# Kernel tuning notes

Hardware: AMD Instinct MI355X
Metric: run time of the kernel (lower is better)

The kernel has to match this reference:

```python
import jax, jax.numpy as jnp
import numpy as np

B, S, D = 8, 1024, 768          # batch, block_size, d_model
H = 6                            # n_head
E = 24                           # n_experts
CAP = 4                          # n_expert_capacity
DH = D // H                      # 128, head dim
DF = 384                         # d_ffn
N = S * H                        # tokens after head split = 6144
K = N * CAP // E                 # tokens per expert = 1024


def _uniform(key, shape, fan_in):
    b = 1.0 / np.sqrt(fan_in)
    return jax.random.uniform(key, shape, jnp.float32, -b, b)


def setup_inputs() -> dict:
    key = jax.random.key(0)
    kx, kc, k1, k2, kh, km = jax.random.split(key, 6)
    return {
        "x": jax.random.normal(kx, (B, S, D), jnp.float32),
        "choice": _uniform(kc, (E, DH), DH),
        "w1": _uniform(k1, (E, DH, DF), DH),
        "w2": _uniform(k2, (E, DF, DH), DF),
        "head": _uniform(kh, (D, D), D),
        "merge": _uniform(km, (D, D), D),
    }


def reference(x, choice, w1, w2, head, merge):
    Bb = x.shape[0]
    # input projection then split heads into a token stream of length N
    x = jnp.einsum("bsd,do->bso", x, head)
    x = x.reshape(Bb, N, DH)                              # [B, N, DH]
    # expert-choice routing: softmax over experts per token
    gates = jax.nn.softmax(jnp.einsum("bsd,ed->bse", x, choice), axis=-1)
    # each expert picks its top-K tokens
    G, I = jax.lax.top_k(jnp.swapaxes(gates, -1, -2), K)  # [B, E, K]
    bidx = jnp.arange(Bb)[:, None, None]
    # gather (equivalent to one-hot matmul einsum('beks,bsd->bekd', P, x))
    x_in = x[bidx, I]                                     # [B, E, K, DH]
    # per-expert SwiGLU-free FFN: silu(x w1) w2
    h = jax.nn.silu(jnp.einsum("bekd,edo->beko", x_in, w1))
    x_mlp = jnp.einsum("beki,eid->bekd", h, w2)           # [B, E, K, DH]
    # scatter-combine weighted by gates (einsum('beks,bek,bekd->bsd'))
    x_out = jnp.zeros((Bb, N, DH), x.dtype).at[bidx, I].add(G[..., None] * x_mlp)
    # dropout is identity in eval mode
    x_out = x_out.reshape(Bb, S, D)
    return jnp.einsum("bsd,do->bso", x_out, merge)
```

## Files before the change

kernel.cpp:

```cpp
#include <hip/hip_runtime.h>
#include <stdint.h>
#include <math.h>

typedef __attribute__((ext_vector_type(8))) short short8;
typedef __attribute__((ext_vector_type(4))) short short4v;
typedef __attribute__((ext_vector_type(4))) float floatx4;

#define DEV static __device__ __forceinline__

DEV float bf2f(unsigned short u){ union { unsigned int i; float f; } c; c.i = ((unsigned int)u) << 16; return c.f; }
DEV unsigned short f2bf(float f){ union { float f; unsigned int i; } c; c.f = f; unsigned int u = c.i; u += 0x7fffu + ((u >> 16) & 1u); return (unsigned short)(u >> 16); }

#if defined(__has_builtin)
#if __has_builtin(__builtin_amdgcn_global_load_lds)
#define USE_GLL 1
#endif
#if __has_builtin(__builtin_amdgcn_exp2f) && __has_builtin(__builtin_amdgcn_rcpf)
#define FAST_SILU 1
#endif
#endif
#ifndef USE_GLL
#define USE_GLL 0
#endif
#ifndef FAST_SILU
#define FAST_SILU 0
#endif

DEV void gll16(const unsigned short* g, unsigned short* ldsbase, int lane){
#if USE_GLL
  __builtin_amdgcn_global_load_lds((const __attribute__((address_space(1))) void*)g,
                                   (__attribute__((address_space(3))) void*)ldsbase, 16, 0, 0);
#else
  *(short8*)(ldsbase + lane * 8) = *(const short8*)g;
#endif
}

DEV float silu(float v){
#if FAST_SILU
  float ex = __builtin_amdgcn_exp2f(v * -1.44269504088896f);
  return v * __builtin_amdgcn_rcpf(1.f + ex);
#else
  return v / (1.f + __expf(-v));
#endif
}

DEV void transpose_tile(const float* in, unsigned short* out, int R, int C,
                        int bx, int by, int bz, int tid, unsigned short* tile)
{
  const long boff = (long)bz * (long)R * (long)C;
  in += boff; out += boff;
  const int c0 = bx * 64, r0 = by * 64;
  const int rr = tid >> 4;
  const int c4 = (tid & 15) * 4;
#pragma unroll
  for (int i = 0; i < 4; i++){
    int r = rr + i * 16;
    floatx4 v = *(const floatx4*)(in + (long)(r0 + r) * C + c0 + c4);
#pragma unroll
    for (int u = 0; u < 4; u++) tile[r * 68 + c4 + u] = f2bf(v[u]);
  }
  __syncthreads();
#pragma unroll
  for (int i = 0; i < 4; i++){
    int cc = rr + i * 16;
    short4v v;
#pragma unroll
    for (int u = 0; u < 4; u++) v[u] = (short)tile[(c4 + u) * 68 + cc];
    *(short4v*)(out + (long)(c0 + cc) * R + r0 + c4) = v;
  }
}

__global__ __launch_bounds__(256) void k_prep(const float* __restrict__ x,
    const float* __restrict__ choice, const float* __restrict__ w1,
    const float* __restrict__ w2, const float* __restrict__ head,
    const float* __restrict__ merge,
    unsigned short* __restrict__ xb, unsigned short* __restrict__ headT,
    unsigned short* __restrict__ mergeT, unsigned short* __restrict__ w1T,
    unsigned short* __restrict__ w2T, double* __restrict__ W64)
{
  __shared__ double buf[1536];
  unsigned short* tile = (unsigned short*)buf;
  const int id = blockIdx.x, tid = threadIdx.x;
  if (id < 144){
    transpose_tile(head, headT, 768, 768, id % 12, id / 12, 0, tid, tile);
  } else if (id < 288){
    int l = id - 144;
    transpose_tile(merge, mergeT, 768, 768, l % 12, l / 12, 0, tid, tile);
  } else if (id < 576){
    int l = id - 288;
    transpose_tile(w1, w1T, 128, 384, l % 6, (l / 6) % 2, l / 12, tid, tile);
  } else if (id < 864){
    int l = id - 576;
    transpose_tile(w2, w2T, 384, 128, l % 2, (l / 2) % 6, l / 12, tid, tile);
  } else if (id < 1248){
    int l = id - 864;
    const int sub = tid >> 7, lt = tid & 127;
    const int d = l * 2 + sub;
    double* hrow = buf + sub * 768;
    for (int i = lt; i < 768; i += 128) hrow[i] = (double)head[(long)d * 768 + i];
    __syncthreads();
    for (int c = lt; c < 144; c += 128){
      int h = c / 24, e = c % 24;
      double a = 0.0;
      const double* hr = hrow + h * 128;
      const float* ch = choice + e * 128;
#pragma unroll 8
      for (int k = 0; k < 128; k++) a += hr[k] * (double)ch[k];
      W64[(long)d * 144 + c] = a;
    }
  } else {
    const long l = id - 1248;
    const long i = (l * 256 + tid) * 4;
    floatx4 v = *(const floatx4*)(x + i);
    short4v o;
#pragma unroll
    for (int u = 0; u < 4; u++) o[u] = (short)f2bf(v[u]);
    *(short4v*)(xb + i) = o;
  }
}

template<int OUTF>
DEV void gemm_body(const unsigned short* __restrict__ A, const unsigned short* __restrict__ BT,
                   unsigned short* __restrict__ C, float* __restrict__ Cf, int N, int K,
                   unsigned short* As, unsigned short* Bs, int m0, int n0, int tid)
{
  const int lane = tid & 63;
  const int w = tid >> 6;
  const int wy = w >> 1, wx = w & 1;

  floatx4 acc[4][4];
  {
    floatx4 z4 = {0.f, 0.f, 0.f, 0.f};
#pragma unroll
    for (int i = 0; i < 4; i++)
#pragma unroll
      for (int j = 0; j < 4; j++) acc[i][j] = z4;
  }

  const int rsub = lane >> 3;
  const int kcol = (lane & 7) * 8;

  for (int k0 = 0; k0 < K; k0 += 64){
#pragma unroll
    for (int i = 0; i < 4; i++){
      const int inst = w * 4 + i;
      const int rr = inst * 8 + rsub;
      gll16(A + (long)(m0 + rr) * K + k0 + kcol, &As[inst * 512], lane);
      gll16(BT + (long)(n0 + rr) * K + k0 + kcol, &Bs[inst * 512], lane);
    }
    __syncthreads();
#pragma unroll
    for (int ks = 0; ks < 2; ++ks){
      const int kb = ks * 32 + (lane >> 4) * 8;
      short8 af[4], bfr[4];
#pragma unroll
      for (int mi = 0; mi < 4; mi++) af[mi]  = *(const short8*)&As[(wy * 64 + mi * 16 + (lane & 15)) * 64 + kb];
#pragma unroll
      for (int ni = 0; ni < 4; ni++) bfr[ni] = *(const short8*)&Bs[(wx * 64 + ni * 16 + (lane & 15)) * 64 + kb];
#pragma unroll
      for (int mi = 0; mi < 4; mi++)
#pragma unroll
        for (int ni = 0; ni < 4; ni++)
          acc[mi][ni] = __builtin_amdgcn_mfma_f32_16x16x32_bf16(af[mi], bfr[ni], acc[mi][ni], 0, 0, 0);
    }
    __syncthreads();
  }

  const int ml = lane & 15;
  const int rq = (lane >> 4) * 4;
#pragma unroll
  for (int mi = 0; mi < 4; mi++){
    const int rowb = m0 + wy * 64 + mi * 16 + rq;
#pragma unroll
    for (int ni = 0; ni < 4; ni++){
      const int col = n0 + wx * 64 + ni * 16 + ml;
#pragma unroll
      for (int r = 0; r < 4; r++){
        float v = acc[mi][ni][r];
        if (OUTF) Cf[(long)(rowb + r) * N + col] = v;
        else      C[(long)(rowb + r) * N + col] = f2bf(v);
      }
    }
  }
}

DEV void gates_body(const float* __restrict__ xg, const double* __restrict__ W,
                    double* __restrict__ P, float* xs, double* Ws,
                    int row0, int ksegIdx, int tid)
{
  const int tx = tid & 15;
  const int ty = tid >> 4;
  const int kseg = ksegIdx * 192;

  double acc[4][9];
#pragma unroll
  for (int i = 0; i < 4; i++)
#pragma unroll
    for (int j = 0; j < 9; j++) acc[i][j] = 0.0;

  for (int kc = 0; kc < 192; kc += 32){
    const int k0 = kseg + kc;
    {
      int rr = tid & 63;
      int kk8 = (tid >> 6) * 8;
      const float* src = xg + (long)(row0 + rr) * 768 + k0 + kk8;
      floatx4 v0 = *(const floatx4*)src;
      floatx4 v1 = *(const floatx4*)(src + 4);
#pragma unroll
      for (int u = 0; u < 4; u++) xs[(kk8 + u) * 64 + rr] = v0[u];
#pragma unroll
      for (int u = 0; u < 4; u++) xs[(kk8 + 4 + u) * 64 + rr] = v1[u];
    }
    for (int f = tid; f < 4608; f += 256) Ws[f] = W[(long)(k0 + f / 144) * 144 + (f % 144)];
    __syncthreads();
#pragma unroll 2
    for (int kk = 0; kk < 32; kk++){
      floatx4 xv = *(const floatx4*)&xs[kk * 64 + ty * 4];
      double xd[4];
#pragma unroll
      for (int i = 0; i < 4; i++) xd[i] = (double)xv[i];
#pragma unroll
      for (int j = 0; j < 9; j++){
        double wv = Ws[kk * 144 + tx + 16 * j];
#pragma unroll
        for (int i = 0; i < 4; i++) acc[i][j] += xd[i] * wv;
      }
    }
    __syncthreads();
  }
  double* dstseg = P + (long)ksegIdx * 8192 * 144;
#pragma unroll
  for (int i = 0; i < 4; i++){
    double* dst = dstseg + (long)(row0 + ty * 4 + i) * 144;
#pragma unroll
    for (int j = 0; j < 9; j++) dst[tx + 16 * j] = acc[i][j];
  }
}

__global__ __launch_bounds__(256, 2) void k_main0(const unsigned short* __restrict__ xb,
    const unsigned short* __restrict__ headT, unsigned short* __restrict__ x1,
    const float* __restrict__ xg, const double* __restrict__ W, double* __restrict__ P)
{
  __shared__ double lds[5632];
  const int id = blockIdx.x, tid = threadIdx.x;
  if (id < 384){
    unsigned short* As = (unsigned short*)lds;
    unsigned short* Bs = As + 128 * 64;
    gemm_body<0>(xb, headT, x1, nullptr, 768, 768, As, Bs, (id & 63) * 128, (id >> 6) * 128, tid);
  } else {
    const int id2 = id - 384;
    float* xs = (float*)lds;
    double* Ws = (double*)((char*)lds + 8192);
    gates_body(xg, W, P, xs, Ws, (id2 & 127) * 64, id2 >> 7, tid);
  }
}

__global__ __launch_bounds__(256) void k_softmax(const double* __restrict__ P,
                                                 double* __restrict__ gatesT)
{
  const int gid = blockIdx.x * 256 + threadIdx.x;
  const int R = gid / 6, h = gid % 6;
  const int b = R >> 10, s = R & 1023;
  const int n = s * 6 + h;
  const long S = (long)8192 * 144;
  const long base = (long)R * 144 + h * 24;
  double l[24];
#pragma unroll
  for (int e = 0; e < 24; e++){
    const long o = base + e;
    l[e] = (P[o] + P[S + o]) + (P[2 * S + o] + P[3 * S + o]);
  }
  double m = l[0];
#pragma unroll
  for (int e = 1; e < 24; e++) m = fmax(m, l[e]);
  double ssum = 0.0;
#pragma unroll
  for (int e = 0; e < 24; e++) ssum += exp(l[e] - m);
  double is = 1.0 / ssum;
#pragma unroll
  for (int e = 0; e < 24; e++)
    gatesT[((long)(b * 24 + e)) * 6144 + n] = exp(l[e] - m) * is;
}

DEV int blk_reduce(int v, volatile int* sbuf, int tid){
#pragma unroll
  for (int off = 32; off > 0; off >>= 1) v += __shfl_down(v, off);
  __syncthreads();
  if ((tid & 63) == 0) sbuf[tid >> 6] = v;
  __syncthreads();
  return sbuf[0] + sbuf[1] + sbuf[2] + sbuf[3];
}

__global__ __launch_bounds__(256) void k_topk(const double* __restrict__ gatesT,
                                              int* __restrict__ Kidx, float* __restrict__ Gval,
                                              int* __restrict__ cnt, unsigned short* __restrict__ inv)
{
  __shared__ int sbuf[4];
  __shared__ int s_pos;
  const int tid = threadIdx.x;
  const int be = blockIdx.x;
  const int b = be / 24, e = be % 24;
  const double* g = gatesT + (long)be * 6144;

  unsigned long long key[24];
#pragma unroll
  for (int j = 0; j < 24; j++)
    key[j] = (unsigned long long)__double_as_longlong(g[tid + 256 * j]);

  unsigned long long lo = 0ull, hi = ~0ull;
  for (int it = 0; it < 64; ++it){
    if (hi - lo <= 1ull) break;
    unsigned long long mid = lo + ((hi - lo) >> 1);
    int c = 0;
#pragma unroll
    for (int j = 0; j < 24; j++) c += (key[j] > mid) ? 1 : 0;
    c = blk_reduce(c, sbuf, tid);
    if (c >= 1024) lo = mid; else hi = mid;
  }
  const unsigned long long T = hi;
  int cg = 0;
#pragma unroll
  for (int j = 0; j < 24; j++) cg += (key[j] > T) ? 1 : 0;
  cg = blk_reduce(cg, sbuf, tid);
  const int need = 1024 - cg;

  int lo2 = 0, hi2 = 6144;
  for (int it = 0; it < 13; ++it){
    if (hi2 - lo2 <= 1) break;
    int mid = (lo2 + hi2) >> 1;
    int c = 0;
#pragma unroll
    for (int j = 0; j < 24; j++) c += (key[j] == T && (tid + 256 * j) < mid) ? 1 : 0;
    c = blk_reduce(c, sbuf, tid);
    if (c >= need) hi2 = mid; else lo2 = mid;
  }
  const int m = hi2;

  if (tid == 0) s_pos = 0;
  __syncthreads();
#pragma unroll
  for (int j = 0; j < 24; j++){
    int n = tid + 256 * j;
    bool sel = (key[j] > T) || (key[j] == T && n < m);
    if (sel){
      int slot = atomicAdd(&s_pos, 1);
      Kidx[(long)be * 1024 + slot] = n;
      Gval[(long)be * 1024 + slot] = (float)__longlong_as_double((long long)key[j]);
      int t = b * 6144 + n;
      int p = atomicAdd(&cnt[t], 1);
      inv[(long)t * 24 + p] = (unsigned short)(e * 1024 + slot);
    }
  }
}

__global__ __launch_bounds__(256, 2) void k_gemm2(const unsigned short* __restrict__ A,
    const unsigned short* __restrict__ BT, float* __restrict__ Cf)
{
  __shared__ unsigned short As[128 * 64];
  __shared__ unsigned short Bs[128 * 64];
  gemm_body<1>(A, BT, nullptr, Cf, 768, 768, As, Bs,
               (int)blockIdx.x * 128, (int)blockIdx.y * 128, (int)threadIdx.x);
}

__global__ __launch_bounds__(256, 2) void k_ffn(const unsigned short* __restrict__ x1,
    const unsigned short* __restrict__ w1T, const unsigned short* __restrict__ w2T,
    const int* __restrict__ KidxAll, const float* __restrict__ GvalAll,
    unsigned short* __restrict__ Y)
{
  __shared__ unsigned short As[128 * 128];
  __shared__ unsigned short W1c[64 * 128];
  __shared__ unsigned short W2c[128 * 64];
  __shared__ unsigned short Hc[128 * 64];
  const int tid = threadIdx.x, lane = tid & 63, w = tid >> 6;
  const int tx = lane & 15, quad = lane >> 4;
  const int mt = blockIdx.x;
  const int be = blockIdx.y;
  const int b = be / 24, e = be % 24;
  const int* idx = KidxAll + (long)be * 1024 + mt * 128;
  const float* scl = GvalAll + (long)be * 1024 + mt * 128;
  const unsigned short* A   = x1  + (long)b * 6144 * 128;
  const unsigned short* w1e = w1T + (long)e * 384 * 128;
  const unsigned short* w2e = w2T + (long)e * 128 * 384;

  {
    const int r0 = w * 32;
#pragma unroll
    for (int i = 0; i < 8; i++){
      int rr = r0 + i * 4 + quad;
      int c = tx ^ (rr & 15);
      gll16(A + (long)idx[rr] * 128 + c * 8, &As[(r0 + i * 4) * 128], lane);
    }
  }

  floatx4 Yt[2][8];
  {
    floatx4 z4 = {0.f, 0.f, 0.f, 0.f};
#pragma unroll
    for (int i = 0; i < 2; i++)
#pragma unroll
      for (int j = 0; j < 8; j++) Yt[i][j] = z4;
  }

  for (int nc = 0; nc < 6; ++nc){
    {
      const int r0 = w * 16;
#pragma unroll
      for (int i = 0; i < 4; i++){
        int lr = r0 + i * 4 + quad;
        int c = tx ^ (lr & 15);
        gll16(w1e + (long)(nc * 64 + lr) * 128 + c * 8, &W1c[(r0 + i * 4) * 128], lane);
      }
    }
    {
      const int r0 = w * 32;
#pragma unroll
      for (int i = 0; i < 4; i++){
        int rr = r0 + i * 8 + (lane >> 3);
        int c = (lane & 7) ^ (rr & 7);
        gll16(w2e + (long)rr * 384 + nc * 64 + c * 8, &W2c[(r0 + i * 8) * 64], lane);
      }
    }
    __syncthreads();

    floatx4 h4[2][4];
    {
      floatx4 z4 = {0.f, 0.f, 0.f, 0.f};
#pragma unroll
      for (int i = 0; i < 2; i++)
#pragma unroll
        for (int j = 0; j < 4; j++) h4[i][j] = z4;
    }
#pragma unroll
    for (int ks = 0; ks < 4; ++ks){
      const int chunk = ks * 4 + quad;
      const int pos = chunk ^ tx;
      short8 af[2];
#pragma unroll
      for (int mi = 0; mi < 2; ++mi)
        af[mi] = *(const short8*)&As[(w * 32 + mi * 16 + tx) * 128 + pos * 8];
#pragma unroll
      for (int nf = 0; nf < 4; ++nf){
        short8 bfr = *(const short8*)&W1c[(nf * 16 + tx) * 128 + pos * 8];
#pragma unroll
        for (int mi = 0; mi < 2; ++mi)
          h4[mi][nf] = __builtin_amdgcn_mfma_f32_16x16x32_bf16(af[mi], bfr, h4[mi][nf], 0, 0, 0);
      }
    }
#pragma unroll
    for (int mi = 0; mi < 2; ++mi){
#pragma unroll
      for (int nf = 0; nf < 4; ++nf){
        const int hchunk = nf * 2 + (tx >> 3);
        const int hoff = tx & 7;
#pragma unroll
        for (int r = 0; r < 4; r++){
          float v = silu(h4[mi][nf][r]);
          const int trow = w * 32 + mi * 16 + quad * 4 + r;
          Hc[trow * 64 + (hchunk ^ (trow & 7)) * 8 + hoff] = f2bf(v);
        }
      }
    }
    __syncthreads();

#pragma unroll
    for (int ks = 0; ks < 2; ++ks){
      const int chunk2 = ks * 4 + quad;
      const int posx = chunk2 ^ (tx & 7);
      short8 a2[2], b2[8];
#pragma unroll
      for (int mf = 0; mf < 2; ++mf)
        a2[mf] = *(const short8*)&W2c[(w * 32 + mf * 16 + tx) * 64 + posx * 8];
#pragma unroll
      for (int nf = 0; nf < 8; ++nf)
        b2[nf] = *(const short8*)&Hc[(nf * 16 + tx) * 64 + posx * 8];
#pragma unroll
      for (int mf = 0; mf < 2; ++mf)
#pragma unroll
        for (int nf = 0; nf < 8; ++nf)
          Yt[mf][nf] = __builtin_amdgcn_mfma_f32_16x16x32_bf16(a2[mf], b2[nf], Yt[mf][nf], 0, 0, 0);
    }
    __syncthreads();
  }

#pragma unroll
  for (int nf = 0; nf < 8; ++nf){
    const int rb = nf * 16 + tx;
    const float g = scl[rb];
    unsigned short* dst = Y + ((long)be * 1024 + mt * 128 + rb) * 128 + w * 32 + quad * 4;
#pragma unroll
    for (int mf = 0; mf < 2; ++mf){
      short4v v;
#pragma unroll
      for (int r = 0; r < 4; r++) v[r] = (short)f2bf(Yt[mf][nf][r] * g);
      *(short4v*)(dst + mf * 16) = v;
    }
  }
}

__global__ __launch_bounds__(256) void k_combine(const int* __restrict__ cnt,
    const unsigned short* __restrict__ inv, const unsigned short* __restrict__ Y,
    unsigned short* __restrict__ xout)
{
  const int t = blockIdx.x * 4 + (threadIdx.x >> 6);
  const int lane = threadIdx.x & 63;
  const int b = t / 6144;
  const int c = cnt[t];
  float a0 = 0.f, a1 = 0.f;
  for (int p = 0; p < c; ++p){
    int code = inv[(long)t * 24 + p];
    int e = code >> 10, slot = code & 1023;
    const unsigned short* y = Y + (((long)(b * 24 + e) * 1024 + slot) << 7) + lane * 2;
    a0 += bf2f(y[0]); a1 += bf2f(y[1]);
  }
  unsigned short* o = xout + ((long)t << 7) + lane * 2;
  o[0] = f2bf(a0); o[1] = f2bf(a1);
}

extern "C" void kernel_launch(void* const* d_in, const int* in_sizes, int n_in,
                              void* d_out, int out_size, void* d_ws, size_t ws_size,
                              hipStream_t stream)
{
  const float* x      = (const float*)d_in[0];
  const float* choice = (const float*)d_in[1];
  const float* w1     = (const float*)d_in[2];
  const float* w2     = (const float*)d_in[3];
  const float* head   = (const float*)d_in[4];
  const float* merge  = (const float*)d_in[5];
  float* out = (float*)d_out;
  (void)in_sizes; (void)n_in; (void)out_size; (void)ws_size;

  char* p = (char*)d_ws;
  auto alloc = [&p](size_t bytes) -> void* {
    void* q = (void*)p; p += (bytes + 255) & ~(size_t)255; return q;
  };

  unsigned short* headT = (unsigned short*)alloc((size_t)768 * 768 * 2);
  unsigned short* mergeT= (unsigned short*)alloc((size_t)768 * 768 * 2);
  unsigned short* w1T   = (unsigned short*)alloc((size_t)24 * 384 * 128 * 2);
  unsigned short* w2T   = (unsigned short*)alloc((size_t)24 * 128 * 384 * 2);
  double* W64           = (double*)alloc((size_t)768 * 144 * 8);
  int* Kidx             = (int*)alloc((size_t)192 * 1024 * 4);
  float* Gval           = (float*)alloc((size_t)192 * 1024 * 4);
  int* cnt              = (int*)alloc((size_t)49152 * 4);
  unsigned short* inv   = (unsigned short*)alloc((size_t)49152 * 24 * 2);
  unsigned short* xb    = (unsigned short*)alloc((size_t)8192 * 768 * 2);
  unsigned short* x1    = (unsigned short*)alloc((size_t)8192 * 768 * 2);
  unsigned short* Y     = (unsigned short*)alloc((size_t)192 * 1024 * 128 * 2);
  double* P             = (double*)Y;
  double* gatesT        = (double*)((char*)Y + (size_t)4 * 8192 * 144 * 8);
  unsigned short* xout  = xb;

  hipMemsetAsync(cnt, 0, (size_t)49152 * 4, stream);
  k_prep<<<dim3(7392), 256, 0, stream>>>(x, choice, w1, w2, head, merge,
                                         xb, headT, mergeT, w1T, w2T, W64);
  k_main0<<<dim3(896), 256, 0, stream>>>(xb, headT, x1, x, W64, P);
  k_softmax<<<dim3(192), 256, 0, stream>>>(P, gatesT);
  k_topk<<<dim3(192), 256, 0, stream>>>(gatesT, Kidx, Gval, cnt, inv);
  k_ffn<<<dim3(8, 192, 1), 256, 0, stream>>>(x1, w1T, w2T, Kidx, Gval, Y);
  k_combine<<<dim3(12288), 256, 0, stream>>>(cnt, inv, Y, xout);
  k_gemm2<<<dim3(64, 6, 1), 256, 0, stream>>>(xout, mergeT, out);
}
```

Before: 390.9 us.

## Restructure fp64 gates GEMM LDS layout, vectorize loads, reorder fused block dispatch

The fp64 gate-logit kernel now stores the x tile row-major with padding, so each thread reads vector float4 rows. The W tile is regrouped so each thread owns 9 contiguous columns, which allows double2 LDS loads and contiguous output stores. The slower gates blocks are now dispatched ahead of the bf16 GEMM blocks in the fused launch to balance the tail. Softmax caches the exp values instead of computing them twice. The output column mapping changes to tx*9+j, which is consistent with how the W tile is regrouped. The LDS footprint grows slightly, which may reduce occupancy.

```diff
diff --git a/kernel.cpp b/kernel.cpp
--- a/kernel.cpp
+++ b/kernel.cpp
@@ -5,6 +5,8 @@
 typedef __attribute__((ext_vector_type(8))) short short8;
 typedef __attribute__((ext_vector_type(4))) short short4v;
 typedef __attribute__((ext_vector_type(4))) float floatx4;
+typedef __attribute__((ext_vector_type(2))) float floatx2;
+typedef __attribute__((ext_vector_type(2))) double doublex2;
 
 #define DEV static __device__ __forceinline__
 
@@ -185,7 +187,7 @@
 }
 
 DEV void gates_body(const float* __restrict__ xg, const double* __restrict__ W,
-                    double* __restrict__ P, float* xs, double* Ws,
+                    double* __restrict__ P, float* xsT , double* Ws ,
                     int row0, int ksegIdx, int tid)
 {
   const int tx = tid & 15;
@@ -201,29 +203,43 @@
   for (int kc = 0; kc < 192; kc += 32){
     const int k0 = kseg + kc;
     {
-      int rr = tid & 63;
-      int kk8 = (tid >> 6) * 8;
-      const float* src = xg + (long)(row0 + rr) * 768 + k0 + kk8;
-      floatx4 v0 = *(const floatx4*)src;
-      floatx4 v1 = *(const floatx4*)(src + 4);
-#pragma unroll
-      for (int u = 0; u < 4; u++) xs[(kk8 + u) * 64 + rr] = v0[u];
-#pragma unroll
-      for (int u = 0; u < 4; u++) xs[(kk8 + 4 + u) * 64 + rr] = v1[u];
-    }
-    for (int f = tid; f < 4608; f += 256) Ws[f] = W[(long)(k0 + f / 144) * 144 + (f % 144)];
-    __syncthreads();
-#pragma unroll 2
-    for (int kk = 0; kk < 32; kk++){
-      floatx4 xv = *(const floatx4*)&xs[kk * 64 + ty * 4];
-      double xd[4];
-#pragma unroll
-      for (int i = 0; i < 4; i++) xd[i] = (double)xv[i];
-#pragma unroll
-      for (int j = 0; j < 9; j++){
-        double wv = Ws[kk * 144 + tx + 16 * j];
-#pragma unroll
-        for (int i = 0; i < 4; i++) acc[i][j] += xd[i] * wv;
+      const int rL = tid >> 4;
+      const int kL = (tid & 15) * 2;
+#pragma unroll
+      for (int p = 0; p < 4; ++p){
+        const int rr = p * 16 + rL;
+        floatx2 v = *(const floatx2*)(xg + (long)(row0 + rr) * 768 + k0 + kL);
+        *(floatx2*)&xsT[rr * 36 + kL] = v;
+      }
+    }
+    for (int f = tid; f < 4608; f += 256){
+      int kk = f / 144, c = f - kk * 144;
+      int c9 = c / 9, cm = c - c9 * 9;
+      Ws[kk * 160 + c9 * 10 + cm] = W[(long)(k0 + kk) * 144 + c];
+    }
+    __syncthreads();
+#pragma unroll
+    for (int q = 0; q < 8; ++q){
+      floatx4 xr[4];
+#pragma unroll
+      for (int i = 0; i < 4; i++)
+        xr[i] = *(const floatx4*)&xsT[(ty * 4 + i) * 36 + q * 4];
+#pragma unroll
+      for (int kk2 = 0; kk2 < 4; ++kk2){
+        const double* wrow = Ws + (q * 4 + kk2) * 160 + tx * 10;
+        double w[9];
+#pragma unroll
+        for (int j2 = 0; j2 < 4; j2++){
+          doublex2 wv = *(const doublex2*)(wrow + j2 * 2);
+          w[j2 * 2] = wv[0]; w[j2 * 2 + 1] = wv[1];
+        }
+        w[8] = wrow[8];
+#pragma unroll
+        for (int i = 0; i < 4; i++){
+          double xd = (double)xr[i][kk2];
+#pragma unroll
+          for (int j = 0; j < 9; j++) acc[i][j] += xd * w[j];
+        }
       }
     }
     __syncthreads();
@@ -231,9 +247,9 @@
   double* dstseg = P + (long)ksegIdx * 8192 * 144;
 #pragma unroll
   for (int i = 0; i < 4; i++){
-    double* dst = dstseg + (long)(row0 + ty * 4 + i) * 144;
-#pragma unroll
-    for (int j = 0; j < 9; j++) dst[tx + 16 * j] = acc[i][j];
+    double* dst = dstseg + (long)(row0 + ty * 4 + i) * 144 + tx * 9;
+#pragma unroll
+    for (int j = 0; j < 9; j++) dst[j] = acc[i][j];
   }
 }
 
@@ -241,17 +257,17 @@
     const unsigned short* __restrict__ headT, unsigned short* __restrict__ x1,
     const float* __restrict__ xg, const double* __restrict__ W, double* __restrict__ P)
 {
-  __shared__ double lds[5632];
+  __shared__ double lds[6272];
   const int id = blockIdx.x, tid = threadIdx.x;
-  if (id < 384){
+  if (id < 512){
+    float* xsT = (float*)lds;
+    double* Ws = (double*)((char*)lds + 9216);
+    gates_body(xg, W, P, xsT, Ws, (id & 127) * 64, id >> 7, tid);
+  } else {
+    const int id2 = id - 512;
     unsigned short* As = (unsigned short*)lds;
     unsigned short* Bs = As + 128 * 64;
-    gemm_body<0>(xb, headT, x1, nullptr, 768, 768, As, Bs, (id & 63) * 128, (id >> 6) * 128, tid);
-  } else {
-    const int id2 = id - 384;
-    float* xs = (float*)lds;
-    double* Ws = (double*)((char*)lds + 8192);
-    gates_body(xg, W, P, xs, Ws, (id2 & 127) * 64, id2 >> 7, tid);
+    gemm_body<0>(xb, headT, x1, nullptr, 768, 768, As, Bs, (id2 & 63) * 128, (id2 >> 6) * 128, tid);
   }
 }
 
@@ -275,11 +291,11 @@
   for (int e = 1; e < 24; e++) m = fmax(m, l[e]);
   double ssum = 0.0;
 #pragma unroll
-  for (int e = 0; e < 24; e++) ssum += exp(l[e] - m);
+  for (int e = 0; e < 24; e++){ l[e] = exp(l[e] - m); ssum += l[e]; }
   double is = 1.0 / ssum;
 #pragma unroll
   for (int e = 0; e < 24; e++)
-    gatesT[((long)(b * 24 + e)) * 6144 + n] = exp(l[e] - m) * is;
+    gatesT[((long)(b * 24 + e)) * 6144 + n] = l[e] * is;
 }
 
 DEV int blk_reduce(int v, volatile int* sbuf, int tid){
```

After: 384.9 us. About the same (-1.5%).
